# Kernel tuning notes

Measured on AMD Instinct MI355X. Metric: run time of the kernel, lower is better.

Reference implementation:

```python
import jax, jax.numpy as jnp
import numpy as np

GRID_RES = 96

TRIANGLE_TABLE = jnp.array([
    [-1, -1, -1, -1, -1, -1], [1, 0, 2, -1, -1, -1], [4, 0, 3, -1, -1, -1], [1, 4, 2, 1, 3, 4],
    [3, 1, 5, -1, -1, -1], [2, 3, 0, 2, 5, 3], [1, 4, 0, 1, 5, 4], [4, 2, 5, -1, -1, -1],
    [4, 5, 2, -1, -1, -1], [4, 1, 0, 4, 5, 1], [3, 2, 0, 3, 5, 2], [1, 3, 5, -1, -1, -1],
    [4, 1, 2, 4, 3, 1], [3, 0, 4, -1, -1, -1], [2, 0, 1, -1, -1, -1], [-1, -1, -1, -1, -1, -1]],
    dtype=jnp.int32)
NUM_TRIANGLES_TABLE = jnp.array([0, 1, 1, 2, 1, 2, 2, 1, 1, 2, 2, 1, 2, 1, 1, 0], dtype=jnp.int32)
BASE_TET_EDGES = jnp.array([0, 1, 0, 2, 0, 3, 1, 2, 1, 3, 2, 3], dtype=jnp.int32)


def _build_tet_grid(R):
    # vertices on an (R+1)^3 lattice spanning [-0.5, 0.5]^3
    n = R + 1
    lin = np.linspace(-0.5, 0.5, n, dtype=np.float32)
    X, Y, Z = np.meshgrid(lin, lin, lin, indexing='ij')
    verts = np.stack([X, Y, Z], axis=-1).reshape(-1, 3)
    idx = np.arange(n ** 3, dtype=np.int32).reshape(n, n, n)
    corners = []
    for dx in (0, 1):
        for dy in (0, 1):
            for dz in (0, 1):
                corners.append(idx[dx:dx + R, dy:dy + R, dz:dz + R].reshape(-1))
    c = np.stack(corners, axis=-1)  # (R^3, 8); corner bit order = dx*4 + dy*2 + dz
    SIX_TETS = np.array([[0, 5, 1, 7], [0, 1, 3, 7], [0, 3, 2, 7],
                         [0, 2, 6, 7], [0, 6, 4, 7], [0, 4, 5, 7]], dtype=np.int32)
    tets = c[:, SIX_TETS].reshape(-1, 4)  # (6*R^3, 4)
    return verts, tets


def _map_uv(face_gidx, max_idx):
    N = int(np.ceil(np.sqrt((max_idx + 1) // 2)))
    lin = jnp.linspace(0.0, 1.0 - 1.0 / N, N, dtype=jnp.float32)
    tex_y, tex_x = jnp.meshgrid(lin, lin, indexing='ij')
    pad = 0.9 / N
    uvs = jnp.stack([tex_x, tex_y, tex_x + pad, tex_y,
                     tex_x + pad, tex_y + pad, tex_x, tex_y + pad], axis=-1).reshape(-1, 2)
    tq = face_gidx // 2
    tet_idx = (tq // N) * N + (tq % N)
    tri_idx = face_gidx % 2
    uv_idx = jnp.stack([tet_idx * 4, tet_idx * 4 + tri_idx + 1, tet_idx * 4 + tri_idx + 2],
                       axis=-1).reshape(-1, 3)
    return uvs, uv_idx


def setup_inputs() -> dict:
    verts_np, tets_np = _build_tet_grid(GRID_RES)
    key = jax.random.key(0)
    verts = jnp.asarray(verts_np)
    noise = jax.random.normal(key, (verts.shape[0],), dtype=jnp.float32) * 0.02
    sdf_n = 0.35 - jnp.linalg.norm(verts, axis=-1) + noise  # sphere SDF + noise
    # 6 features per vertex: deformed position (xyz) + color (rgb=0.5), as in getMesh
    pos_nx3 = jnp.concatenate([verts, jnp.full(verts.shape, 0.5, dtype=jnp.float32)], axis=-1)
    return {"pos_nx3": pos_nx3, "sdf_n": sdf_n, "tet_fx4": jnp.asarray(tets_np)}


def reference(pos_nx3, sdf_n, tet_fx4):
    occ_n = sdf_n >= 0
    occ_fx4 = occ_n[tet_fx4]                       # (F, 4)
    occ_sum = occ_fx4.sum(-1)
    valid = (occ_sum > 0) & (occ_sum < 4)
    vt = tet_fx4[valid]                            # (T, 4) surface-crossing tets

    all_edges = vt[:, BASE_TET_EDGES].reshape(-1, 2)
    all_edges = jnp.sort(all_edges, axis=1)        # == sort_edges (min, max)
    unique_edges, idx_map = jnp.unique(all_edges, axis=0, return_inverse=True)
    idx_map = idx_map.reshape(-1)

    mask_edges = occ_n[unique_edges].sum(-1) == 1  # sign-crossing edges
    # mapping[mask] = arange(num_crossing); else -1 (cumsum assigns in sorted order)
    mapping = jnp.where(mask_edges, jnp.cumsum(mask_edges.astype(jnp.int32)) - 1, -1)
    idx_map = mapping[idx_map].reshape(-1, 6)      # (T, 6)
    interp_v = unique_edges[mask_edges]            # (Nv, 2)

    e_pos = pos_nx3[interp_v]                      # (Nv, 2, 6)
    e_sdf = sdf_n[interp_v] * jnp.array([1.0, -1.0], dtype=sdf_n.dtype)  # negate 2nd
    denom = e_sdf.sum(1, keepdims=True)            # (Nv, 1)
    w = jnp.flip(e_sdf, axis=1) / denom            # (Nv, 2) interpolation weights
    verts = (e_pos * w[..., None]).sum(1)          # (Nv, 6)

    v_id = jnp.array([1, 2, 4, 8], dtype=jnp.int32)
    tetindex = (occ_fx4[valid].astype(jnp.int32) * v_id).sum(-1)
    num_tri = NUM_TRIANGLES_TABLE[tetindex]
    tt = TRIANGLE_TABLE[tetindex]
    m1 = num_tri == 1
    m2 = num_tri == 2
    faces1 = jnp.take_along_axis(idx_map[m1], tt[m1][:, :3], axis=1).reshape(-1, 3)
    faces2 = jnp.take_along_axis(idx_map[m2], tt[m2][:, :6], axis=1).reshape(-1, 3)
    faces = jnp.concatenate([faces1, faces2], axis=0)

    num_tets = tet_fx4.shape[0]
    tet_gidx = jnp.arange(num_tets, dtype=jnp.int32)[valid]
    g2 = tet_gidx[m2] * 2
    face_gidx = jnp.concatenate([tet_gidx[m1] * 2,
                                 jnp.stack([g2, g2 + 1], axis=-1).reshape(-1)], axis=0)
    uvs, uv_idx = _map_uv(face_gidx, num_tets * 2)
    return verts, faces, uvs, uv_idx
```

## Files before the change

kernel.cpp:

```cpp
#include <hip/hip_runtime.h>
#include <stdint.h>

#define N1     97
#define N1SQ   9409
#define NV3    912673
#define RES    96
#define NCELL  884736
#define NCOLS  9409
#define COLS_PER_BLK 8
#define NBLK1  1177
#define SEG    2
#define UVFLOATS 42467328

#define VB2 3566
#define FB2 3456
#define NSPARSE (VB2 + FB2)
#define UVB2 10368
#define P2BLOCKS (2 * NSPARSE + (UVB2 - NSPARSE))

typedef float f4v __attribute__((ext_vector_type(4)));

__device__ __constant__ int d_tt[16][6] = {
    {-1,-1,-1,-1,-1,-1}, {1,0,2,-1,-1,-1}, {4,0,3,-1,-1,-1}, {1,4,2,1,3,4},
    {3,1,5,-1,-1,-1}, {2,3,0,2,5,3}, {1,4,0,1,5,4}, {4,2,5,-1,-1,-1},
    {4,5,2,-1,-1,-1}, {4,1,0,4,5,1}, {3,2,0,3,5,2}, {1,3,5,-1,-1,-1},
    {4,1,2,4,3,1}, {3,0,4,-1,-1,-1}, {2,0,1,-1,-1,-1}, {-1,-1,-1,-1,-1,-1}};
__device__ __constant__ int d_six[6][4] = {
    {0,5,1,7},{0,1,3,7},{0,3,2,7},{0,2,6,7},{0,6,4,7},{0,4,5,7}};
__device__ __constant__ int d_eb[6][2] = {{0,1},{0,2},{0,3},{1,2},{1,3},{2,3}};
__device__ __constant__ int d_diroff[7] = {1, 97, 98, 9409, 9410, 9506, 9507};

__device__ __forceinline__ int corner_off(int b) {
    return (b >> 2) * N1SQ + ((b >> 1) & 1) * N1 + (b & 1);
}

__device__ __forceinline__ float uvval(uint32_t p) {
    uint32_t cell = p >> 3;
    uint32_t k = p & 7u;
    uint32_t i = cell / 2304u;
    uint32_t j = cell - i * 2304u;
    uint32_t idx = (k & 1u) ? i : j;
    bool addpad = (k & 1u) ? (k >= 5u) : (k == 2u || k == 4u);
    return (float)idx * (1.0f / 2304.0f) + (addpad ? 0.9f / 2304.0f : 0.0f);
}

__global__ __launch_bounds__(1024) void k_p1(const float* __restrict__ sdf,
                                             uint32_t* __restrict__ mvl,
                                             uint32_t* __restrict__ vsums,
                                             uint8_t* __restrict__ cocc,
                                             uint32_t* __restrict__ cloc,
                                             uint64_t* __restrict__ csums) {
    __shared__ uint8_t  sgn[COLS_PER_BLK][128];
    __shared__ uint64_t wtc[16];
    int t = threadIdx.x;
    int lane = t & 63, wv = t >> 6;
    int bid = blockIdx.x;
    int sub = t >> 7, z = t & 127;
    int col = bid * COLS_PER_BLK + sub;
    bool vcol = col < NCOLS;
    int x = 0, y = 0;
    if (vcol) { x = col / N1; y = col - x * N1; }
    bool bx = x < RES, by = y < RES, bz = z < RES;
    bool vact = vcol && (z < N1);
    int b00 = col * N1;
    float f00 = 0.f, f01 = 0.f, f10 = 0.f, f11 = 0.f;
    if (vact) {
        f00 = sdf[b00 + z];
        if (by) f01 = sdf[b00 + N1 + z];
        if (bx) f10 = sdf[b00 + N1SQ + z];
        if (bx && by) f11 = sdf[b00 + N1SQ + N1 + z];
    }
    uint32_t sb = (f00 >= 0.f ? 1u : 0u) | (f01 >= 0.f ? 2u : 0u) |
                  (f10 >= 0.f ? 4u : 0u) | (f11 >= 0.f ? 8u : 0u);
    sgn[sub][z] = (uint8_t)sb;
    __syncthreads();
    uint32_t s1 = bz ? (uint32_t)sgn[sub][z + 1] : 0u;

    uint32_t o0 = sb & 1u;
    uint32_t vm = 0;
    if (vact) {
        if (bz && ((s1 & 1u) != o0)) vm |= 1u;
        if (by && (((sb >> 1) & 1u) != o0)) vm |= 2u;
        if (by && bz && (((s1 >> 1) & 1u) != o0)) vm |= 4u;
        if (bx && (((sb >> 2) & 1u) != o0)) vm |= 8u;
        if (bx && bz && (((s1 >> 2) & 1u) != o0)) vm |= 16u;
        if (bx && by && (((sb >> 3) & 1u) != o0)) vm |= 32u;
        if (bx && by && bz && (((s1 >> 3) & 1u) != o0)) vm |= 64u;
    }
    uint32_t cnt = __popc(vm);
    bool cact = vact && bx && by && bz;
    uint32_t occ = 0, m1 = 0, m2 = 0;
    if (cact) {
        occ = (sb & 1u) | ((s1 & 1u) << 1) | (((sb >> 1) & 1u) << 2) | (((s1 >> 1) & 1u) << 3) |
              (((sb >> 2) & 1u) << 4) | (((s1 >> 2) & 1u) << 5) |
              (((sb >> 3) & 1u) << 6) | (((s1 >> 3) & 1u) << 7);
        if (occ != 0u && occ != 255u) {
#pragma unroll
            for (int k = 0; k < 6; k++) {
                int ti = ((occ >> d_six[k][0]) & 1) | (((occ >> d_six[k][1]) & 1) << 1) |
                         (((occ >> d_six[k][2]) & 1) << 2) | (((occ >> d_six[k][3]) & 1) << 3);
                int pc = __popc((uint32_t)ti);
                m1 += (pc == 1 || pc == 3) ? 1u : 0u;
                m2 += (pc == 2) ? 1u : 0u;
            }
        }
    }
    uint64_t val = (uint64_t)(cnt | (m1 << 16)) | ((uint64_t)m2 << 32);
    unsigned long long incl = val;
#pragma unroll
    for (int d = 1; d < 64; d <<= 1) {
        unsigned long long u = __shfl_up(incl, d, 64);
        if (lane >= d) incl += u;
    }
    if (lane == 63) wtc[wv] = incl;
    __syncthreads();
    uint64_t pre = 0;
#pragma unroll
    for (int w = 0; w < 16; w++)
        if (w < wv) pre += wtc[w];
    uint64_t excl = pre + (uint64_t)incl - val;

    if (vact) {
        mvl[b00 + z] = ((uint32_t)(excl & 0xffffu) << 8) | vm;
    }
    if (cact) {
        int c = (x * RES + y) * RES + z;
        cocc[c] = (uint8_t)occ;
        cloc[c] = (uint32_t)((excl >> 16) & 0xffffu) | ((uint32_t)((excl >> 32) & 0xffffu) << 16);
    }
    if (t == 0) {
        uint64_t btot = 0;
#pragma unroll
        for (int w = 0; w < 16; w++) btot += wtc[w];
        vsums[bid] = (uint32_t)(btot & 0xffffu);
        csums[bid] = ((btot >> 16) & 0xffffu) | (((btot >> 32) & 0xffffu) << 32);
    }
}

__global__ __launch_bounds__(1024) void k_sums2(uint32_t* __restrict__ vsums,
                                                uint64_t* __restrict__ csums,
                                                uint32_t* __restrict__ tot) {
    __shared__ uint32_t wtv[16];
    __shared__ uint64_t wtc[16];
    int t = threadIdx.x;
    int lane = t & 63, wv = t >> 6;
    uint32_t sv = 0; uint64_t sc = 0;
    int base = t * SEG;
#pragma unroll
    for (int j = 0; j < SEG; j++) {
        int idx = base + j;
        if (idx < NBLK1) { sv += vsums[idx]; sc += csums[idx]; }
    }
    uint32_t iv = sv; unsigned long long ic = sc;
#pragma unroll
    for (int d = 1; d < 64; d <<= 1) {
        uint32_t u1 = __shfl_up(iv, d, 64);
        unsigned long long u2 = __shfl_up(ic, d, 64);
        if (lane >= d) { iv += u1; ic += u2; }
    }
    if (lane == 63) { wtv[wv] = iv; wtc[wv] = ic; }
    __syncthreads();
    uint32_t pv = 0; uint64_t pc2 = 0;
#pragma unroll
    for (int w = 0; w < 16; w++)
        if (w < wv) { pv += wtv[w]; pc2 += wtc[w]; }
    uint32_t rv = pv + iv - sv;
    uint64_t rc = pc2 + (uint64_t)ic - sc;
#pragma unroll
    for (int j = 0; j < SEG; j++) {
        int idx = base + j;
        if (idx < NBLK1) {
            uint32_t a = vsums[idx]; uint64_t b = csums[idx];
            vsums[idx] = rv; csums[idx] = rc;
            rv += a; rc += b;
        }
    }
    if (t == 0) {
        uint32_t NV = 0; uint64_t tc = 0;
#pragma unroll
        for (int w = 0; w < 16; w++) { NV += wtv[w]; tc += wtc[w]; }
        uint32_t NF1 = (uint32_t)(tc & 0xffffffffu);
        uint32_t NF2 = (uint32_t)(tc >> 32);
        uint32_t NF  = NF1 + 2u * NF2;
        tot[0] = NV; tot[1] = NF1; tot[2] = NF2;
        tot[3] = NV * 6u;
        tot[4] = NV * 6u + NF * 3u;
        tot[5] = NV * 6u + NF * 3u + UVFLOATS;
    }
}

__global__ __launch_bounds__(256) void k_p2(const float* __restrict__ sdf,
                                            const float* __restrict__ pos,
                                            const uint32_t* __restrict__ mvl,
                                            const uint32_t* __restrict__ vsums,
                                            const uint8_t* __restrict__ cocc,
                                            const uint32_t* __restrict__ cloc,
                                            const uint64_t* __restrict__ csums,
                                            const uint32_t* __restrict__ tot,
                                            float* __restrict__ out) {
    __shared__ uint2 ls[4][768];
    int bid = blockIdx.x;
    int t = threadIdx.x;
    int lane = t & 63, wv = t >> 6;
    int sparse = -1, uvb = -1;
    if (bid < 2 * NSPARSE) {
        if (bid & 1) uvb = bid >> 1;
        else sparse = bid >> 1;
    } else {
        uvb = NSPARSE + (bid - 2 * NSPARSE);
    }

    if (uvb >= 0) {
        uint32_t tot4 = tot[4];
        uint32_t A = (tot4 + 31u) & ~31u;
        uint32_t end = tot4 + UVFLOATS;
        uint32_t nvec = (end - A) >> 2;
        uint32_t vi0 = (uint32_t)uvb * 1024u + (uint32_t)t;
        uint32_t p0 = (A - tot4) + vi0 * 4u;
        uint32_t cell = p0 >> 3;
        uint32_t ph4 = p0 & 4u;
        uint32_t i = cell / 2304u;
        uint32_t j = cell - i * 2304u;
        const float s = 1.0f / 2304.0f, pd = 0.9f / 2304.0f;
#pragma unroll
        for (int rr = 0; rr < 4; rr++) {
            uint32_t vi = vi0 + (uint32_t)rr * 256u;
            if (vi < nvec) {
                float xx = (float)j * s, yy = (float)i * s;
                f4v val;
                if (ph4) { val.x = xx + pd; val.y = yy + pd; val.z = xx;      val.w = yy + pd; }
                else     { val.x = xx;      val.y = yy;      val.z = xx + pd; val.w = yy; }
                *(f4v*)(out + A + (size_t)vi * 4u) = val;
            }
            j += 128u;
            if (j >= 2304u) { j -= 2304u; i += 1u; }
        }
        if (uvb == 0 && t == 0) {
            for (uint32_t e = tot4; e < A; e++) out[e] = uvval(e - tot4);
            for (uint32_t e = A + nvec * 4u; e < end; e++) out[e] = uvval(e - tot4);
        }
        return;
    }

    if (sparse < VB2) {
        int v = sparse * 256 + wv * 64 + lane;
        uint32_t mv = (v < NV3) ? mvl[v] : 0u;
        uint32_t m = mv & 0xffu;
        uint32_t cnt = __popc(m);
        uint32_t incl = cnt;
#pragma unroll
        for (int d = 1; d < 64; d <<= 1) {
            uint32_t u = __shfl_up(incl, d, 64);
            if (lane >= d) incl += u;
        }
        uint32_t E = __shfl(incl, 63);
        if (E == 0) return;
        uint32_t slot = incl - cnt;
        if (cnt) {
            uint32_t gvid = (mv >> 8) + vsums[(v / N1) >> 3];
#pragma unroll
            for (int d = 0; d < 7; d++) {
                if ((m >> d) & 1u) {
                    ls[wv][slot] = make_uint2((uint32_t)v, (gvid << 3) | (uint32_t)d);
                    gvid++; slot++;
                }
            }
        }
        for (uint32_t j = lane; j < E; j += 64) {
            uint2 e = ls[wv][j];
            uint32_t v0 = e.x;
            uint32_t dir = e.y & 7u;
            uint32_t vid = e.y >> 3;
            uint32_t b = v0 + (uint32_t)d_diroff[dir];
            float sa = sdf[v0];
            float sbv = sdf[b];
            float inv = 1.0f / (sa - sbv);
            float w0 = -sbv * inv;
            float w1 = sa * inv;
            const float2* pa2 = (const float2*)(pos + (size_t)v0 * 6);
            const float2* pb2 = (const float2*)(pos + (size_t)b * 6);
            float2* o2 = (float2*)(out + (size_t)vid * 6);
#pragma unroll
            for (int k = 0; k < 3; k++) {
                float2 a = pa2[k], bb = pb2[k];
                float2 o;
                o.x = a.x * w0 + bb.x * w1;
                o.y = a.y * w0 + bb.y * w1;
                o2[k] = o;
            }
        }
        return;
    }

    {
        int c = (sparse - VB2) * 256 + wv * 64 + lane;
        uint32_t occ = cocc[c];
        bool valid = (occ != 0u && occ != 255u);
        uint32_t NF1 = tot[1];
        uint32_t tis = 0, nts = 0, cnt = 0;
        if (valid) {
#pragma unroll
            for (int k = 0; k < 6; k++) {
                int ti = ((occ >> d_six[k][0]) & 1) | (((occ >> d_six[k][1]) & 1) << 1) |
                         (((occ >> d_six[k][2]) & 1) << 2) | (((occ >> d_six[k][3]) & 1) << 3);
                int pc = __popc((uint32_t)ti);
                int nt = (pc == 2) ? 2 : ((pc == 1 || pc == 3) ? 1 : 0);
                tis |= (uint32_t)ti << (4 * k);
                nts |= (uint32_t)nt << (2 * k);
                cnt += (uint32_t)nt;
            }
        }
        uint32_t incl = cnt;
#pragma unroll
        for (int d = 1; d < 64; d <<= 1) {
            uint32_t u = __shfl_up(incl, d, 64);
            if (lane >= d) incl += u;
        }
        uint32_t E = __shfl(incl, 63);
        if (E == 0) return;
        uint32_t slot = incl - cnt;
        if (cnt) {
            uint32_t cl = cloc[c];
            uint64_t cs = csums[(((c / (RES * RES)) * N1) + ((c / RES) % RES)) >> 3];
            uint32_t r1 = (uint32_t)(cs & 0xffffffffu) + (cl & 0xffffu);
            uint32_t r2 = (uint32_t)(cs >> 32) + (cl >> 16);
#pragma unroll 1
            for (int k = 0; k < 6; k++) {
                uint32_t nt = (nts >> (2 * k)) & 3u;
                if (!nt) continue;
                uint32_t ti = (tis >> (4 * k)) & 15u;
                uint32_t row0;
                if (nt == 1) { row0 = r1; r1++; }
                else         { row0 = NF1 + 2u * r2; r2++; }
                for (uint32_t tri = 0; tri < nt; tri++) {
                    ls[wv][slot] = make_uint2((uint32_t)c,
                        ((row0 + tri) << 8) | (ti << 4) | ((uint32_t)k << 1) | tri);
                    slot++;
                }
            }
        }
        uint32_t fbase = tot[3];
        uint32_t ubase = tot[5];
        for (uint32_t j = lane; j < E; j += 64) {
            uint2 e = ls[wv][j];
            uint32_t cc = e.x;
            uint32_t tri = e.y & 1u;
            uint32_t k = (e.y >> 1) & 7u;
            uint32_t ti = (e.y >> 4) & 15u;
            uint32_t rr = e.y >> 8;
            uint32_t cx = cc / (RES * RES);
            uint32_t r0 = cc - cx * (RES * RES);
            uint32_t cy = r0 / RES;
            uint32_t cz = r0 - cy * RES;
            int base = (int)(cx * N1SQ + cy * N1 + cz);
            float* f = out + (size_t)fbase + (size_t)rr * 3;
            float* u = out + (size_t)ubase + (size_t)rr * 3;
#pragma unroll
            for (int jj = 0; jj < 3; jj++) {
                int ee = d_tt[ti][tri * 3 + jj];
                int c0 = d_six[k][d_eb[ee][0]];
                int c1 = d_six[k][d_eb[ee][1]];
                int bl = c0 & c1;
                int rank = (c0 ^ c1) - 1;
                int v0 = base + corner_off(bl);
                uint32_t mvlv = mvl[v0];
                uint32_t vid = (mvlv >> 8) + vsums[(v0 / N1) >> 3] +
                               (uint32_t)__popc((mvlv & 0xffu) & ((1u << rank) - 1u));
                f[jj] = (float)vid;
            }
            uint32_t t_g = cc * 6u + k;
            u[0] = (float)(4u * t_g);
            u[1] = (float)(4u * t_g + tri + 1u);
            u[2] = (float)(4u * t_g + tri + 2u);
        }
    }
}

extern "C" void kernel_launch(void* const* d_in, const int* in_sizes, int n_in,
                              void* d_out, int out_size, void* d_ws, size_t ws_size,
                              hipStream_t stream) {
    const float* pos = (const float*)d_in[0];
    const float* sdf = (const float*)d_in[1];
    float* out = (float*)d_out;

    uint8_t* ws = (uint8_t*)d_ws;
    size_t off = 0;
    auto alloc = [&](size_t bytes) {
        void* p = ws + off;
        off = (off + bytes + 255) & ~(size_t)255;
        return p;
    };
    uint32_t* tot   = (uint32_t*)alloc(64);
    uint32_t* mvl   = (uint32_t*)alloc((size_t)NV3 * 4);
    uint32_t* vsums = (uint32_t*)alloc((size_t)NBLK1 * 4);
    uint8_t*  cocc  = (uint8_t*)alloc(NCELL);
    uint32_t* cloc  = (uint32_t*)alloc((size_t)NCELL * 4);
    uint64_t* csums = (uint64_t*)alloc((size_t)NBLK1 * 8);

    hipLaunchKernelGGL(k_p1, dim3(NBLK1), dim3(1024), 0, stream,
                       sdf, mvl, vsums, cocc, cloc, csums);
    hipLaunchKernelGGL(k_sums2, dim3(1), dim3(1024), 0, stream, vsums, csums, tot);
    hipLaunchKernelGGL(k_p2, dim3(P2BLOCKS), dim3(256), 0, stream,
                       sdf, pos, mvl, vsums, cocc, cloc, csums, tot, out);
}
```

Before: 56.97 us.

## Split fused phase-2 kernel into separate UV-fill and sparse kernels

Splits the combined phase-2 kernel, which interleaved UV-writing blocks with sparse vertex/face blocks, into two kernels launched back to back. The UV kernel now writes 16 vectors per thread instead of 4, so it needs far fewer blocks. The sparse kernel no longer carries the 6 KB shared-memory footprint onto UV blocks or branches on block type. The cost is an extra launch and the loss of overlap between the bandwidth-bound UV stores and the latency-bound sparse work.

```diff
diff --git a/kernel.cpp b/kernel.cpp
--- a/kernel.cpp
+++ b/kernel.cpp
@@ -15,8 +15,7 @@
 #define VB2 3566
 #define FB2 3456
 #define NSPARSE (VB2 + FB2)
-#define UVB2 10368
-#define P2BLOCKS (2 * NSPARSE + (UVB2 - NSPARSE))
+#define UVBLKS 2593
 
 typedef float f4v __attribute__((ext_vector_type(4)));
 
@@ -189,61 +188,55 @@
     }
 }
 
-__global__ __launch_bounds__(256) void k_p2(const float* __restrict__ sdf,
-                                            const float* __restrict__ pos,
-                                            const uint32_t* __restrict__ mvl,
-                                            const uint32_t* __restrict__ vsums,
-                                            const uint8_t* __restrict__ cocc,
-                                            const uint32_t* __restrict__ cloc,
-                                            const uint64_t* __restrict__ csums,
-                                            const uint32_t* __restrict__ tot,
-                                            float* __restrict__ out) {
+__global__ __launch_bounds__(256) void k_uvs(const uint32_t* __restrict__ tot,
+                                             float* __restrict__ out) {
+    int t = threadIdx.x;
+    uint32_t tot4 = tot[4];
+    uint32_t A = (tot4 + 31u) & ~31u;
+    uint32_t end = tot4 + UVFLOATS;
+    uint32_t nvec = (end - A) >> 2;
+    uint32_t vi0 = (uint32_t)blockIdx.x * 4096u + (uint32_t)t;
+    uint32_t p0 = (A - tot4) + vi0 * 4u;
+    uint32_t cell = p0 >> 3;
+    uint32_t ph4 = p0 & 4u;
+    uint32_t i = cell / 2304u;
+    uint32_t j = cell - i * 2304u;
+    const float s = 1.0f / 2304.0f, pd = 0.9f / 2304.0f;
+#pragma unroll
+    for (int rr = 0; rr < 16; rr++) {
+        uint32_t vi = vi0 + (uint32_t)rr * 256u;
+        if (vi < nvec) {
+            float xx = (float)j * s, yy = (float)i * s;
+            f4v val;
+            if (ph4) { val.x = xx + pd; val.y = yy + pd; val.z = xx;      val.w = yy + pd; }
+            else     { val.x = xx;      val.y = yy;      val.z = xx + pd; val.w = yy; }
+            *(f4v*)(out + A + (size_t)vi * 4u) = val;
+        }
+        j += 128u;
+        if (j >= 2304u) { j -= 2304u; i += 1u; }
+    }
+    if (blockIdx.x == 0 && t == 0) {
+        for (uint32_t e = tot4; e < A; e++) out[e] = uvval(e - tot4);
+        for (uint32_t e = A + nvec * 4u; e < end; e++) out[e] = uvval(e - tot4);
+    }
+}
+
+__global__ __launch_bounds__(256) void k_sparse(const float* __restrict__ sdf,
+                                                const float* __restrict__ pos,
+                                                const uint32_t* __restrict__ mvl,
+                                                const uint32_t* __restrict__ vsums,
+                                                const uint8_t* __restrict__ cocc,
+                                                const uint32_t* __restrict__ cloc,
+                                                const uint64_t* __restrict__ csums,
+                                                const uint32_t* __restrict__ tot,
+                                                float* __restrict__ out) {
     __shared__ uint2 ls[4][768];
-    int bid = blockIdx.x;
+    int sp = blockIdx.x;
     int t = threadIdx.x;
     int lane = t & 63, wv = t >> 6;
-    int sparse = -1, uvb = -1;
-    if (bid < 2 * NSPARSE) {
-        if (bid & 1) uvb = bid >> 1;
-        else sparse = bid >> 1;
-    } else {
-        uvb = NSPARSE + (bid - 2 * NSPARSE);
-    }
-
-    if (uvb >= 0) {
-        uint32_t tot4 = tot[4];
-        uint32_t A = (tot4 + 31u) & ~31u;
-        uint32_t end = tot4 + UVFLOATS;
-        uint32_t nvec = (end - A) >> 2;
-        uint32_t vi0 = (uint32_t)uvb * 1024u + (uint32_t)t;
-        uint32_t p0 = (A - tot4) + vi0 * 4u;
-        uint32_t cell = p0 >> 3;
-        uint32_t ph4 = p0 & 4u;
-        uint32_t i = cell / 2304u;
-        uint32_t j = cell - i * 2304u;
-        const float s = 1.0f / 2304.0f, pd = 0.9f / 2304.0f;
-#pragma unroll
-        for (int rr = 0; rr < 4; rr++) {
-            uint32_t vi = vi0 + (uint32_t)rr * 256u;
-            if (vi < nvec) {
-                float xx = (float)j * s, yy = (float)i * s;
-                f4v val;
-                if (ph4) { val.x = xx + pd; val.y = yy + pd; val.z = xx;      val.w = yy + pd; }
-                else     { val.x = xx;      val.y = yy;      val.z = xx + pd; val.w = yy; }
-                *(f4v*)(out + A + (size_t)vi * 4u) = val;
-            }
-            j += 128u;
-            if (j >= 2304u) { j -= 2304u; i += 1u; }
-        }
-        if (uvb == 0 && t == 0) {
-            for (uint32_t e = tot4; e < A; e++) out[e] = uvval(e - tot4);
-            for (uint32_t e = A + nvec * 4u; e < end; e++) out[e] = uvval(e - tot4);
-        }
-        return;
-    }
-
-    if (sparse < VB2) {
-        int v = sparse * 256 + wv * 64 + lane;
+
+    if (sp < VB2) {
+        int v = sp * 256 + wv * 64 + lane;
         uint32_t mv = (v < NV3) ? mvl[v] : 0u;
         uint32_t m = mv & 0xffu;
         uint32_t cnt = __popc(m);
@@ -293,7 +286,7 @@
     }
 
     {
-        int c = (sparse - VB2) * 256 + wv * 64 + lane;
+        int c = (sp - VB2) * 256 + wv * 64 + lane;
         uint32_t occ = cocc[c];
         bool valid = (occ != 0u && occ != 255u);
         uint32_t NF1 = tot[1];
@@ -400,6 +393,7 @@
     hipLaunchKernelGGL(k_p1, dim3(NBLK1), dim3(1024), 0, stream,
                        sdf, mvl, vsums, cocc, cloc, csums);
     hipLaunchKernelGGL(k_sums2, dim3(1), dim3(1024), 0, stream, vsums, csums, tot);
-    hipLaunchKernelGGL(k_p2, dim3(P2BLOCKS), dim3(256), 0, stream,
+    hipLaunchKernelGGL(k_uvs, dim3(UVBLKS), dim3(256), 0, stream, tot, out);
+    hipLaunchKernelGGL(k_sparse, dim3(NSPARSE), dim3(256), 0, stream,
                        sdf, pos, mvl, vsums, cocc, cloc, csums, tot, out);
 }
```

After: 67.32 us. 1.18x slower.
